# Kernel tuning notes

Measured on AMD Instinct MI355X. Metric: run time of the kernel, lower is better.

The kernel has to match this reference:

```python
import jax, jax.numpy as jnp
import numpy as np

B, T, S, L = 1, 2048, 512, 1024
C, H, Hk, D = 2048, 16, 4, 128
THETA = 10000.0


def setup_inputs() -> dict:
    key = jax.random.key(0)
    ks = jax.random.split(key, 9)
    sd = 0.02
    return {
        "x": jax.random.normal(ks[0], (B, T, C), jnp.float32),
        "stm": jax.random.normal(ks[1], (B, S, C), jnp.float32),
        "long_q": jax.random.normal(ks[2], (B, L, H, D), jnp.float32),
        "long_k": jax.random.normal(ks[3], (B, L, Hk, D), jnp.float32),
        "long_v": jax.random.normal(ks[4], (B, L, Hk, D), jnp.float32),
        "Wq": jax.random.normal(ks[5], (C, C), jnp.float32) * sd,
        "Wk": jax.random.normal(ks[6], (C, Hk * D), jnp.float32) * sd,
        "Wv": jax.random.normal(ks[7], (C, Hk * D), jnp.float32) * sd,
        "Wo": jax.random.normal(ks[8], (C, C), jnp.float32) * sd,
    }


def _rope_cos_sin(n, d, theta):
    # precompute_freqs_cis: freqs over even dims, angles t*freq
    freqs = 1.0 / (theta ** (jnp.arange(0, d, 2, dtype=jnp.float32) / d))
    ang = jnp.arange(n, dtype=jnp.float32)[:, None] * freqs[None, :]  # (n, d/2)
    return jnp.cos(ang), jnp.sin(ang)


def _apply_rope(x, cos, sin):
    # x: (B, n, h, D); complex-pair rotation over consecutive dims
    x1, x2 = x[..., 0::2], x[..., 1::2]
    c = cos[None, :, None, :]
    s = sin[None, :, None, :]
    r1 = x1 * c - x2 * s
    r2 = x1 * s + x2 * c
    return jnp.stack([r1, r2], axis=-1).reshape(x.shape)


def reference(x, stm, long_q, long_k, long_v, Wq, Wk, Wv, Wo):
    Bb, Tt, Cc = x.shape
    Ss, Ll = stm.shape[1], long_q.shape[1]
    seq = jnp.concatenate([stm, x], axis=1)  # (B, S+T, C)
    q = jnp.concatenate([long_q, (seq @ Wq).reshape(Bb, Ss + Tt, H, D)], axis=1)
    k = jnp.concatenate([long_k, (seq @ Wk).reshape(Bb, Ss + Tt, Hk, D)], axis=1)
    v = jnp.concatenate([long_v, (seq @ Wv).reshape(Bb, Ss + Tt, Hk, D)], axis=1)
    # inline RoPE on the last T+S positions only (memory bank keeps fixed encoding)
    cos, sin = _rope_cos_sin(Ss + Tt, D, THETA)
    q = q.at[:, Ll:].set(_apply_rope(q[:, Ll:], cos, sin))
    k = k.at[:, Ll:].set(_apply_rope(k[:, Ll:], cos, sin))
    tot = Ll + Ss + Tt
    # structured memory mask: causal over full stream, memory keys (< L+S) visible to all
    idx = jnp.arange(tot)
    mask = (idx[None, :] <= idx[:, None]) | (idx[None, :] < Ll + Ss)  # (tot, tot)
    # GQA: repeat_interleave kv heads
    rep = H // Hk
    kr = jnp.repeat(k, rep, axis=2)  # (B, tot, H, D)
    vr = jnp.repeat(v, rep, axis=2)
    att = jnp.einsum("bihd,bjhd->bhij", q, kr) * (1.0 / np.sqrt(D))
    att = jnp.where(mask[None, None], att, -jnp.inf)
    att = jax.nn.softmax(att, axis=-1)
    y = jnp.einsum("bhij,bjhd->bihd", att, vr).reshape(Bb, tot, Cc)
    y = y[:, -Tt:]  # keep only current-block outputs
    return y @ Wo
```

## Files before the change

kernel.cpp:

```cpp
#include <hip/hip_runtime.h>
#include <hip/hip_bf16.h>

typedef __attribute__((ext_vector_type(8))) short short8;
typedef __attribute__((ext_vector_type(4))) short short4v;
typedef __attribute__((ext_vector_type(4))) float f32x4;
typedef __attribute__((ext_vector_type(4))) float float4v;
typedef __attribute__((ext_vector_type(4))) int i32x4;

#define DEVFN static __device__ __forceinline__

#define T_N   2048
#define S_N   512
#define L_N   1024
#define C_N   2048
#define H_N   16
#define HK_N  4
#define D_N   128
#define ST_N  2560
#define TOT_N 3584
#define KV_N  512

DEVFN short f2bf(float f) {
  union { float f; unsigned u; } v; v.f = f;
  return (short)((v.u + 0x7FFFu + ((v.u >> 16) & 1u)) >> 16);
}
DEVFN float bf2f(short s) {
  union { unsigned u; float f; } v; v.u = ((unsigned)(unsigned short)s) << 16;
  return v.f;
}
DEVFN void gload16(const void* g, void* l) {
  __builtin_amdgcn_global_load_lds(
      (__attribute__((address_space(1))) void*)(g),
      (__attribute__((address_space(3))) void*)(l), 16, 0, 0);
}

#define Q_A (S_N * C_N / 4)
#define Q_B (Q_A + T_N * C_N / 4)
#define Q_C (Q_B + L_N * KV_N / 4)
#define Q_D (Q_C + L_N * KV_N / 4)
#define TAB_E (Q_D + ST_N * 64)
__global__ void k_setup(const float* __restrict__ x, const float* __restrict__ stm,
                        const float* __restrict__ lk, const float* __restrict__ lv,
                        short* __restrict__ seq, short* __restrict__ Kf,
                        short* __restrict__ Vf, float* __restrict__ ct,
                        float* __restrict__ st_) {
  int i = blockIdx.x * 256 + threadIdx.x;
  if (i < Q_D) {
    const float* src; short* dst; int off;
    if (i < Q_A)      { src = stm; dst = seq;                         off = i; }
    else if (i < Q_B) { src = x;   dst = seq + (size_t)S_N * C_N;     off = i - Q_A; }
    else if (i < Q_C) { src = lk;  dst = Kf;                          off = i - Q_B; }
    else              { src = lv;  dst = Vf;                          off = i - Q_C; }
    float4v v = reinterpret_cast<const float4v*>(src)[off];
    short4v o;
    o[0] = f2bf(v[0]); o[1] = f2bf(v[1]); o[2] = f2bf(v[2]); o[3] = f2bf(v[3]);
    reinterpret_cast<short4v*>(dst)[off] = o;
  } else {
    int j = i - Q_D;
    int p = j >> 6, fq = j & 63;
    float freq = expf(-(float)fq * (logf(10000.0f) / 64.0f));
    float ang = (float)p * freq;
    ct[j] = cosf(ang);
    st_[j] = sinf(ang);
  }
}

__global__ void k_tconv_all(const float* __restrict__ Wq, const float* __restrict__ Wk,
                            const float* __restrict__ Wv, const float* __restrict__ Wo,
                            short* __restrict__ WqT, short* __restrict__ WkT,
                            short* __restrict__ WvT, short* __restrict__ WoT) {
  __shared__ float tile[32][33];
  const int z = blockIdx.z;
  const float* in = (z == 0) ? Wq : (z == 1) ? Wk : (z == 2) ? Wv : Wo;
  short* outp     = (z == 0) ? WqT : (z == 1) ? WkT : (z == 2) ? WvT : WoT;
  const int cols = (z == 1 || z == 2) ? KV_N : C_N;
  if (blockIdx.x * 32 >= cols) return;
  int c0 = blockIdx.x * 32, r0 = blockIdx.y * 32;
  int tx = threadIdx.x, ty = threadIdx.y;
#pragma unroll
  for (int i = 0; i < 4; i++)
    tile[ty + i * 8][tx] = in[(size_t)(r0 + ty + i * 8) * cols + c0 + tx];
  __syncthreads();
#pragma unroll
  for (int i = 0; i < 4; i++)
    outp[(size_t)(c0 + ty + i * 8) * C_N + r0 + tx] = f2bf(tile[tx][ty + i * 8]);
}

__global__ void k_tv(const short* __restrict__ vf, short* __restrict__ vt) {
  __shared__ short tile[32][33];
  int hk = blockIdx.z;
  int r0 = blockIdx.x * 32;
  int d0 = blockIdx.y * 32;
  int tx = threadIdx.x, ty = threadIdx.y;
#pragma unroll
  for (int i = 0; i < 4; i++)
    tile[ty + i * 8][tx] = vf[(size_t)(r0 + ty + i * 8) * KV_N + hk * D_N + d0 + tx];
  __syncthreads();
  short* o = vt + (size_t)hk * D_N * TOT_N;
#pragma unroll
  for (int i = 0; i < 4; i++)
    o[(size_t)(d0 + ty + i * 8) * TOT_N + r0 + tx] = tile[tx][ty + i * 8];
}

__global__ __launch_bounds__(256) void k_gemm_o(
    const short* __restrict__ A, const short* __restrict__ Bt,
    float* __restrict__ C) {
  __shared__ short lbuf[2 * 6144];
  const int tid = threadIdx.x;
  const int w = tid >> 6, l = tid & 63;
  const int l15 = l & 15, lh = l >> 4;
  const int f0 = blockIdx.x;
  const int f = ((f0 & 7) << 6) + (f0 >> 3);
  const int rb = (f >> 4) << 6, cb = (f & 15) << 7;
  const int wr = (w >> 1) << 5, wc = (w & 1) << 6;
  f32x4 acc[2][4] = {};
  const int cA = tid;
  const short* pa = &A[(size_t)(rb + (cA >> 2)) * 2048 + (((cA ^ (cA >> 2)) & 3) << 3)];
  const int cB0 = tid, cB1 = 256 + tid;
  const short* pb0 = &Bt[(size_t)(cb + (cB0 >> 2)) * 2048 + (((cB0 ^ (cB0 >> 2)) & 3) << 3)];
  const short* pb1 = &Bt[(size_t)(cb + (cB1 >> 2)) * 2048 + (((cB1 ^ (cB1 >> 2)) & 3) << 3)];
  const int offA  = (w * 64) << 4;
  const int offB0 = 4096 + ((w * 64) << 4);
  const int offB1 = 4096 + ((256 + w * 64) << 4);
  char* lbase = (char*)lbuf;
  const int sw = (lh ^ (l15 & 3)) << 3;
  gload16(pa,  lbase + offA);
  gload16(pb0, lbase + offB0);
  gload16(pb1, lbase + offB1);
  int cur = 0;
  for (int kt = 0; kt < 2048; kt += 32) {
    const bool more = (kt + 32 < 2048);
    if (more) {
      char* p = lbase + (cur ^ 1) * 12288;
      gload16(pa  + kt + 32, p + offA);
      gload16(pb0 + kt + 32, p + offB0);
      gload16(pb1 + kt + 32, p + offB1);
      asm volatile("s_waitcnt vmcnt(3)" ::: "memory");
    } else {
      asm volatile("s_waitcnt vmcnt(0)" ::: "memory");
    }
    __builtin_amdgcn_s_barrier();
    __builtin_amdgcn_sched_barrier(0);
    const short* la = (const short*)(lbase + cur * 12288);
    const short* lb = (const short*)(lbase + cur * 12288 + 4096);
    short8 af[2], bg[4];
#pragma unroll
    for (int m = 0; m < 2; m++)
      af[m] = *reinterpret_cast<const short8*>(&la[(wr + m * 16 + l15) * 32 + sw]);
#pragma unroll
    for (int n = 0; n < 4; n++)
      bg[n] = *reinterpret_cast<const short8*>(&lb[(wc + n * 16 + l15) * 32 + sw]);
    __builtin_amdgcn_s_setprio(1);
#pragma unroll
    for (int m = 0; m < 2; m++)
#pragma unroll
      for (int n = 0; n < 4; n++)
        acc[m][n] = __builtin_amdgcn_mfma_f32_16x16x32_bf16(af[m], bg[n], acc[m][n], 0, 0, 0);
    __builtin_amdgcn_s_setprio(0);
    asm volatile("s_waitcnt lgkmcnt(0)" ::: "memory");
    __builtin_amdgcn_sched_barrier(0);
    __builtin_amdgcn_s_barrier();
    __builtin_amdgcn_sched_barrier(0);
    cur ^= 1;
  }
#pragma unroll
  for (int m = 0; m < 2; m++)
#pragma unroll
    for (int n = 0; n < 4; n++)
#pragma unroll
      for (int r = 0; r < 4; r++) {
        int row = rb + wr + m * 16 + lh * 4 + r;
        int col = cb + wc + n * 16 + l15;
        C[(size_t)row * 2048 + col] = acc[m][n][r];
      }
}

__global__ __launch_bounds__(256) void k_gemm_qkv(
    const short* __restrict__ A, const short* __restrict__ Bt,
    short* __restrict__ qbuf, short* __restrict__ Kf, short* __restrict__ Vf,
    const float* __restrict__ ct, const float* __restrict__ st_) {
  const int Kd = C_N;
  __shared__ short lbuf[2 * 2 * 4096];
  const int tid = threadIdx.x;
  const int w = tid >> 6, l = tid & 63;
  const int l15 = l & 15, lh = l >> 4;
  const int f0 = blockIdx.x;
  const int f = (f0 % 8) * 52 + f0 / 8;
  int rb, cb;
  if (f < 256) {
    rb = 512 + ((f >> 4) << 7);
    cb = (f & 15) << 7;
  } else {
    int g = f - 256;
    rb = (g >> 3) << 7;
    cb = 2048 + ((g & 7) << 7);
  }
  const int wr = (w >> 1) << 6, wc = (w & 1) << 6;
  f32x4 acc[4][4] = {};
  const int c0 = tid, c1 = 256 + tid;
  const short* pa0 = &A[(size_t)(rb + (c0 >> 2)) * Kd + (((c0 ^ (c0 >> 2)) & 3) << 3)];
  const short* pa1 = &A[(size_t)(rb + (c1 >> 2)) * Kd + (((c1 ^ (c1 >> 2)) & 3) << 3)];
  const short* pb0 = &Bt[(size_t)(cb + (c0 >> 2)) * Kd + (((c0 ^ (c0 >> 2)) & 3) << 3)];
  const short* pb1 = &Bt[(size_t)(cb + (c1 >> 2)) * Kd + (((c1 ^ (c1 >> 2)) & 3) << 3)];
  const int offA0 = (w * 64) << 4, offA1 = ((256 + w * 64) << 4);
  char* lbase = (char*)lbuf;
  const int sw = (lh ^ (l15 & 3)) << 3;
  {
    gload16(pa0, lbase + offA0);
    gload16(pa1, lbase + offA1);
    gload16(pb0, lbase + 8192 + offA0);
    gload16(pb1, lbase + 8192 + offA1);
  }
  int cur = 0;
  for (int kt = 0; kt < Kd; kt += 32) {
    const bool more = (kt + 32 < Kd);
    if (more) {
      char* p = lbase + ((cur ^ 1) << 14);
      gload16(pa0 + kt + 32, p + offA0);
      gload16(pa1 + kt + 32, p + offA1);
      gload16(pb0 + kt + 32, p + 8192 + offA0);
      gload16(pb1 + kt + 32, p + 8192 + offA1);
      asm volatile("s_waitcnt vmcnt(4)" ::: "memory");
    } else {
      asm volatile("s_waitcnt vmcnt(0)" ::: "memory");
    }
    __builtin_amdgcn_s_barrier();
    __builtin_amdgcn_sched_barrier(0);
    const short* la = (const short*)(lbase + (cur << 14));
    const short* lb = (const short*)(lbase + (cur << 14) + 8192);
    short8 af[4], bg[4];
#pragma unroll
    for (int m = 0; m < 4; m++)
      af[m] = *reinterpret_cast<const short8*>(&la[(wr + m * 16 + l15) * 32 + sw]);
#pragma unroll
    for (int n = 0; n < 4; n++)
      bg[n] = *reinterpret_cast<const short8*>(&lb[(wc + n * 16 + l15) * 32 + sw]);
    __builtin_amdgcn_s_setprio(1);
#pragma unroll
    for (int m = 0; m < 4; m++)
#pragma unroll
      for (int n = 0; n < 4; n++)
        acc[m][n] = __builtin_amdgcn_mfma_f32_16x16x32_bf16(af[m], bg[n], acc[m][n], 0, 0, 0);
    __builtin_amdgcn_s_setprio(0);
    asm volatile("s_waitcnt lgkmcnt(0)" ::: "memory");
    __builtin_amdgcn_sched_barrier(0);
    __builtin_amdgcn_s_barrier();
    __builtin_amdgcn_sched_barrier(0);
    cur ^= 1;
  }
#pragma unroll
  for (int m = 0; m < 4; m++)
#pragma unroll
    for (int n = 0; n < 4; n++) {
      int coln = cb + wc + n * 16 + l15;
      const bool do_rope = coln < 2560;
      const int fidx = (coln & 127) >> 1;
#pragma unroll
      for (int r = 0; r < 4; r++) {
        int row = rb + wr + m * 16 + lh * 4 + r;
        float v = acc[m][n][r];
        float other = __shfl_xor(v, 1, 64);
        if (do_rope) {
          float co = ct[row * 64 + fidx];
          float si = st_[row * 64 + fidx];
          v = (l15 & 1) ? (other * si + v * co) : (v * co - other * si);
        }
        short bv = f2bf(v);
        if (coln < 2048) {
          if (row >= 512) qbuf[(size_t)(row - 512) * C_N + coln] = bv;
        } else if (coln < 2560) {
          Kf[(size_t)(L_N + row) * KV_N + (coln - 2048)] = bv;
        } else {
          Vf[(size_t)(L_N + row) * KV_N + (coln - 2560)] = bv;
        }
      }
    }
}

__global__ __launch_bounds__(256, 2) void k_attn(
    const short* __restrict__ Q,
    const short* __restrict__ Kf,
    const short* __restrict__ Vt,
    short* __restrict__ pY,
    float* __restrict__ pM,
    float* __restrict__ pL) {
  __shared__ short kl[64 * 128];
  __shared__ short vl[128 * 64];
  const int f = blockIdx.x;
  const int p = f >> 8;
  const int f8 = f & 255;
  const int hk = f8 & 3;
  const int qraw = (f8 >> 2) & 15;
  const int hh = (f8 >> 6) & 3;
  const int qb = p ? (15 - qraw) : qraw;
  const int h = hk * 4 + hh;
  const int tid = threadIdx.x, w = tid >> 6, l = tid & 63;
  const int l15 = l & 15, lh = l >> 4;
  const int qbase = qb << 7;
  const int qrow0 = qbase + (w << 5);
  short8 aqA[4], aqB[4];
#pragma unroll
  for (int kb = 0; kb < 4; kb++) {
    aqA[kb] = *reinterpret_cast<const short8*>(
        &Q[(size_t)(qrow0 + l15) * C_N + h * D_N + kb * 32 + lh * 8]);
    aqB[kb] = *reinterpret_cast<const short8*>(
        &Q[(size_t)(qrow0 + 16 + l15) * C_N + h * D_N + kb * 32 + lh * 8]);
  }
  short8 ones;
#pragma unroll
  for (int j = 0; j < 8; j++) ones[j] = (short)0x3F80;
  f32x4 yA[8] = {}, yB[8] = {};
  f32x4 lA_ = {}, lB_ = {};
  float mA = -3.0e38f, mB = -3.0e38f;
  const float K2 = 0.12751744f;
  const float THR = 90.0f;
  const int nkt = ((qbase + 1663) >> 6) + 1;
  const int th = nkt >> 1;
  const int t0 = p ? th : 0;
  const int t1 = p ? nkt : th;
  const short* psk[4];
  const short* psv[4];
  int ldsoff[4];
#pragma unroll
  for (int it = 0; it < 4; it++) {
    int c = it * 256 + tid;
    int kr = c >> 4, kkc = c & 15;
    int pkr = (kr & 0x23) | ((kr & 0x0C) << 1) | ((kr >> 2) & 4);
    psk[it] = &Kf[(size_t)pkr * KV_N + hk * D_N + ((kkc ^ (kr & 7)) << 3)];
    int vrow = c >> 3, vkc = c & 7;
    psv[it] = &Vt[(size_t)hk * D_N * TOT_N + (size_t)vrow * TOT_N + ((vkc ^ (vrow & 7)) << 3)];
    ldsoff[it] = (it * 256 + w * 64) << 4;
  }
#pragma unroll
  for (int it = 0; it < 4; it++)
    gload16(psk[it] + (size_t)t0 * 64 * KV_N, (char*)kl + ldsoff[it]);
#pragma unroll
  for (int it = 0; it < 4; it++)
    gload16(psv[it] + (size_t)t0 * 64, (char*)vl + ldsoff[it]);
  __syncthreads();
  for (int t = t0; t < t1; t++) {
    const bool more = (t + 1 < t1);
    short8 kreg[4], vreg[4];
    if (more) {
#pragma unroll
      for (int it = 0; it < 4; it++)
        kreg[it] = *reinterpret_cast<const short8*>(psk[it] + (size_t)(t + 1) * 64 * KV_N);
#pragma unroll
      for (int it = 0; it < 4; it++)
        vreg[it] = *reinterpret_cast<const short8*>(psv[it] + (size_t)(t + 1) * 64);
    }
    f32x4 sA[4] = {}, sB[4] = {};
    __builtin_amdgcn_s_setprio(1);
#pragma unroll
    for (int g = 0; g < 4; g++) {
      int row = g * 16 + l15;
#pragma unroll
      for (int kb = 0; kb < 4; kb++) {
        short8 bk = *reinterpret_cast<const short8*>(
            (const char*)kl + row * 256 + ((((kb << 2) + lh) ^ (row & 7)) << 4));
        sA[g] = __builtin_amdgcn_mfma_f32_16x16x32_bf16(bk, aqA[kb], sA[g], 0, 0, 0);
        sB[g] = __builtin_amdgcn_mfma_f32_16x16x32_bf16(bk, aqB[kb], sB[g], 0, 0, 0);
      }
    }
    __builtin_amdgcn_s_setprio(0);
    if ((t * 64 + 63) > (1536 + qrow0)) {
      int qi = qrow0 + l15;
#pragma unroll
      for (int g = 0; g < 4; g++)
#pragma unroll
        for (int r = 0; r < 4; r++) {
          int key = t * 64 + ((g >> 1) << 5) + (lh << 3) + ((g & 1) << 2) + r;
          if (key > 1536 + qi) sA[g][r] = -3.0e38f;
        }
    }
    if ((t * 64 + 63) > (1536 + qrow0 + 16)) {
      int qi = qrow0 + 16 + l15;
#pragma unroll
      for (int g = 0; g < 4; g++)
#pragma unroll
        for (int r = 0; r < 4; r++) {
          int key = t * 64 + ((g >> 1) << 5) + (lh << 3) + ((g & 1) << 2) + r;
          if (key > 1536 + qi) sB[g][r] = -3.0e38f;
        }
    }
    {
      float lm = sA[0][0];
#pragma unroll
      for (int g = 0; g < 4; g++)
#pragma unroll
        for (int r = 0; r < 4; r++) lm = fmaxf(lm, sA[g][r]);
      if (!__all(lm <= mA + THR)) {
        float rm = fmaxf(lm, __shfl_xor(lm, 16, 64));
        rm = fmaxf(rm, __shfl_xor(rm, 32, 64));
        float mn = fmaxf(mA, rm);
        float scf = __builtin_amdgcn_exp2f((mA - mn) * K2);
        mA = mn;
#pragma unroll
        for (int r = 0; r < 4; r++) {
          float sc_c = __shfl(scf, lh * 4 + r, 64);
          lA_[r] *= sc_c;
#pragma unroll
          for (int dg = 0; dg < 8; dg++) yA[dg][r] *= sc_c;
        }
      }
    }
    {
      float lm = sB[0][0];
#pragma unroll
      for (int g = 0; g < 4; g++)
#pragma unroll
        for (int r = 0; r < 4; r++) lm = fmaxf(lm, sB[g][r]);
      if (!__all(lm <= mB + THR)) {
        float rm = fmaxf(lm, __shfl_xor(lm, 16, 64));
        rm = fmaxf(rm, __shfl_xor(rm, 32, 64));
        float mn = fmaxf(mB, rm);
        float scf = __builtin_amdgcn_exp2f((mB - mn) * K2);
        mB = mn;
#pragma unroll
        for (int r = 0; r < 4; r++) {
          float sc_c = __shfl(scf, lh * 4 + r, 64);
          lB_[r] *= sc_c;
#pragma unroll
          for (int dg = 0; dg < 8; dg++) yB[dg][r] *= sc_c;
        }
      }
    }
    union { i32x4 wv; short8 sv; } uA0, uA1, uB0, uB1;
    {
      const float mk = mA * K2;
      float pvv[16];
#pragma unroll
      for (int g = 0; g < 4; g++)
#pragma unroll
        for (int r = 0; r < 4; r++)
          pvv[g * 4 + r] = __builtin_amdgcn_exp2f(sA[g][r] * K2 - mk);
#pragma unroll
      for (int j = 0; j < 4; j++) {
        unsigned w0, w1;
        int b0 = (j >> 1) * 4 + 2 * (j & 1);
        int b1 = (2 + (j >> 1)) * 4 + 2 * (j & 1);
        asm("v_cvt_pk_bf16_f32 %0, %1, %2" : "=v"(w0) : "v"(pvv[b0]), "v"(pvv[b0 + 1]));
        asm("v_cvt_pk_bf16_f32 %0, %1, %2" : "=v"(w1) : "v"(pvv[b1]), "v"(pvv[b1 + 1]));
        uA0.wv[j] = (int)w0;
        uA1.wv[j] = (int)w1;
      }
    }
    {
      const float mk = mB * K2;
      float pvv[16];
#pragma unroll
      for (int g = 0; g < 4; g++)
#pragma unroll
        for (int r = 0; r < 4; r++)
          pvv[g * 4 + r] = __builtin_amdgcn_exp2f(sB[g][r] * K2 - mk);
#pragma unroll
      for (int j = 0; j < 4; j++) {
        unsigned w0, w1;
        int b0 = (j >> 1) * 4 + 2 * (j & 1);
        int b1 = (2 + (j >> 1)) * 4 + 2 * (j & 1);
        asm("v_cvt_pk_bf16_f32 %0, %1, %2" : "=v"(w0) : "v"(pvv[b0]), "v"(pvv[b0 + 1]));
        asm("v_cvt_pk_bf16_f32 %0, %1, %2" : "=v"(w1) : "v"(pvv[b1]), "v"(pvv[b1 + 1]));
        uB0.wv[j] = (int)w0;
        uB1.wv[j] = (int)w1;
      }
    }
    lA_ = __builtin_amdgcn_mfma_f32_16x16x32_bf16(uA0.sv, ones, lA_, 0, 0, 0);
    lA_ = __builtin_amdgcn_mfma_f32_16x16x32_bf16(uA1.sv, ones, lA_, 0, 0, 0);
    lB_ = __builtin_amdgcn_mfma_f32_16x16x32_bf16(uB0.sv, ones, lB_, 0, 0, 0);
    lB_ = __builtin_amdgcn_mfma_f32_16x16x32_bf16(uB1.sv, ones, lB_, 0, 0, 0);
    __builtin_amdgcn_s_setprio(1);
#pragma unroll
    for (int dg = 0; dg < 8; dg++) {
      int vrow = dg * 16 + l15;
      short8 bv0 = *reinterpret_cast<const short8*>(
          (const char*)vl + (vrow << 7) + ((lh ^ (vrow & 7)) << 4));
      short8 bv1 = *reinterpret_cast<const short8*>(
          (const char*)vl + (vrow << 7) + (((4 + lh) ^ (vrow & 7)) << 4));
      yA[dg] = __builtin_amdgcn_mfma_f32_16x16x32_bf16(uA0.sv, bv0, yA[dg], 0, 0, 0);
      yA[dg] = __builtin_amdgcn_mfma_f32_16x16x32_bf16(uA1.sv, bv1, yA[dg], 0, 0, 0);
      yB[dg] = __builtin_amdgcn_mfma_f32_16x16x32_bf16(uB0.sv, bv0, yB[dg], 0, 0, 0);
      yB[dg] = __builtin_amdgcn_mfma_f32_16x16x32_bf16(uB1.sv, bv1, yB[dg], 0, 0, 0);
    }
    __builtin_amdgcn_s_setprio(0);
    asm volatile("s_waitcnt lgkmcnt(0)" ::: "memory");
    __builtin_amdgcn_sched_barrier(0);
    __builtin_amdgcn_s_barrier();
    __builtin_amdgcn_sched_barrier(0);
    if (more) {
#pragma unroll
      for (int it = 0; it < 4; it++)
        *reinterpret_cast<short8*>((char*)kl + ldsoff[it] + (l << 4)) = kreg[it];
#pragma unroll
      for (int it = 0; it < 4; it++)
        *reinterpret_cast<short8*>((char*)vl + ldsoff[it] + (l << 4)) = vreg[it];
    }
    __syncthreads();
  }
  const size_t base = (size_t)(p * 16 + h) * 2048;
#pragma unroll
  for (int dg = 0; dg < 8; dg++)
#pragma unroll
    for (int r = 0; r < 4; r++) {
      int rowA = qrow0 + lh * 4 + r;
      pY[(base + rowA) * 128 + dg * 16 + l15] = f2bf(yA[dg][r]);
      pY[(base + rowA + 16) * 128 + dg * 16 + l15] = f2bf(yB[dg][r]);
    }
  if (l15 == 0) {
#pragma unroll
    for (int r = 0; r < 4; r++) {
      pL[base + qrow0 + lh * 4 + r] = lA_[r];
      pL[base + qrow0 + 16 + lh * 4 + r] = lB_[r];
    }
  }
  if (lh == 0) {
    pM[base + qrow0 + l15] = mA;
    pM[base + qrow0 + 16 + l15] = mB;
  }
}

__global__ void k_merge(const short* __restrict__ pY, const float* __restrict__ pM,
                        const float* __restrict__ pL, short* __restrict__ Y) {
  const int h = blockIdx.y;
  const int row = blockIdx.x * 16 + (threadIdx.x >> 4);
  const int d0 = (threadIdx.x & 15) * 8;
  const size_t b0 = (size_t)h * 2048 + row;
  const size_t b1 = (size_t)(16 + h) * 2048 + row;
  const float K2 = 0.12751744f;
  float m0 = pM[b0], m1 = pM[b1];
  float l0 = pL[b0], l1 = pL[b1];
  float M = fmaxf(m0, m1);
  float a0 = __builtin_amdgcn_exp2f((m0 - M) * K2);
  float a1 = __builtin_amdgcn_exp2f((m1 - M) * K2);
  float inv = 1.0f / (l0 * a0 + l1 * a1);
  short8 y0 = *reinterpret_cast<const short8*>(&pY[b0 * 128 + d0]);
  short8 y1 = *reinterpret_cast<const short8*>(&pY[b1 * 128 + d0]);
  short8 o;
#pragma unroll
  for (int j = 0; j < 8; j++)
    o[j] = f2bf((bf2f(y0[j]) * a0 + bf2f(y1[j]) * a1) * inv);
  *reinterpret_cast<short8*>(&Y[(size_t)row * C_N + h * D_N + d0]) = o;
}

extern "C" void kernel_launch(void* const* d_in, const int* in_sizes, int n_in,
                              void* d_out, int out_size, void* d_ws, size_t ws_size,
                              hipStream_t stream) {
  const float* x      = (const float*)d_in[0];
  const float* stm    = (const float*)d_in[1];
  const float* long_k = (const float*)d_in[3];
  const float* long_v = (const float*)d_in[4];
  const float* Wq     = (const float*)d_in[5];
  const float* Wk     = (const float*)d_in[6];
  const float* Wv     = (const float*)d_in[7];
  const float* Wo     = (const float*)d_in[8];
  float* out = (float*)d_out;

  short* seq  = (short*)d_ws;
  short* WqT  = seq  + (size_t)ST_N * C_N;
  short* WkT  = WqT  + (size_t)C_N * C_N;
  short* WvT  = WkT  + (size_t)KV_N * C_N;
  short* WoT  = WvT  + (size_t)KV_N * C_N;
  short* qbuf = WoT  + (size_t)C_N * C_N;
  short* Kf   = qbuf + (size_t)T_N * C_N;
  short* Vf   = Kf   + (size_t)TOT_N * KV_N;
  short* Vt   = Vf   + (size_t)TOT_N * KV_N;
  short* ybuf = Vt   + (size_t)TOT_N * KV_N;
  float* ctab = (float*)(ybuf + (size_t)T_N * C_N);
  float* stab = ctab + (size_t)ST_N * 64;

  short* pY = (short*)d_ws;
  float* pM = (float*)(pY + (size_t)2 * 16 * 2048 * 128);
  float* pL = pM + (size_t)2 * 16 * 2048;

  k_setup<<<TAB_E / 256, 256, 0, stream>>>(x, stm, long_k, long_v, seq, Kf, Vf, ctab, stab);

  k_tconv_all<<<dim3(64, 64, 4), dim3(32, 8), 0, stream>>>(
      Wq, Wk, Wv, Wo, WqT, WkT, WvT, WoT);

  k_gemm_qkv<<<416, 256, 0, stream>>>(seq, WqT, qbuf, Kf, Vf, ctab, stab);

  k_tv<<<dim3(TOT_N / 32, D_N / 32, HK_N), dim3(32, 8), 0, stream>>>(Vf, Vt);

  k_attn<<<512, 256, 0, stream>>>(qbuf, Kf, Vt, pY, pM, pL);

  k_merge<<<dim3(128, 16), 256, 0, stream>>>(pY, pM, pL, ybuf);

  k_gemm_o<<<512, 256, 0, stream>>>(ybuf, WoT, out);
}
```

Baseline: 169.3 us.

## Split attention KV range four ways and merge four partial softmax results

The attention kernel now divides each query block's key tiles into four chunks instead of two, launching 1024 blocks, and the merge kernel combines four partial outputs using their max and sum statistics. The launch bound is raised to allow four blocks per CU. Two of the partial output buffers are placed in the output buffer as scratch, because the output is only written later by the O-projection GEMM. More blocks gives better load balance and occupancy, at the cost of more partial-result traffic, a heavier merge, and possible register spills under the tighter launch bound.

```diff
diff --git a/kernel.cpp b/kernel.cpp
--- a/kernel.cpp
+++ b/kernel.cpp
@@ -277,11 +277,12 @@
     }
 }
 
-__global__ __launch_bounds__(256, 2) void k_attn(
+__global__ __launch_bounds__(256, 4) void k_attn(
     const short* __restrict__ Q,
     const short* __restrict__ Kf,
     const short* __restrict__ Vt,
-    short* __restrict__ pY,
+    short* __restrict__ pYa,
+    short* __restrict__ pYb,
     float* __restrict__ pM,
     float* __restrict__ pL) {
   __shared__ short kl[64 * 128];
@@ -292,7 +293,7 @@
   const int hk = f8 & 3;
   const int qraw = (f8 >> 2) & 15;
   const int hh = (f8 >> 6) & 3;
-  const int qb = p ? (15 - qraw) : qraw;
+  const int qb = (p & 1) ? (15 - qraw) : qraw;
   const int h = hk * 4 + hh;
   const int tid = threadIdx.x, w = tid >> 6, l = tid & 63;
   const int l15 = l & 15, lh = l >> 4;
@@ -315,9 +316,8 @@
   const float K2 = 0.12751744f;
   const float THR = 90.0f;
   const int nkt = ((qbase + 1663) >> 6) + 1;
-  const int th = nkt >> 1;
-  const int t0 = p ? th : 0;
-  const int t1 = p ? nkt : th;
+  const int tb = (p * nkt) >> 2;
+  const int te = ((p + 1) * nkt) >> 2;
   const short* psk[4];
   const short* psv[4];
   int ldsoff[4];
@@ -333,13 +333,13 @@
   }
 #pragma unroll
   for (int it = 0; it < 4; it++)
-    gload16(psk[it] + (size_t)t0 * 64 * KV_N, (char*)kl + ldsoff[it]);
+    gload16(psk[it] + (size_t)tb * 64 * KV_N, (char*)kl + ldsoff[it]);
 #pragma unroll
   for (int it = 0; it < 4; it++)
-    gload16(psv[it] + (size_t)t0 * 64, (char*)vl + ldsoff[it]);
+    gload16(psv[it] + (size_t)tb * 64, (char*)vl + ldsoff[it]);
   __syncthreads();
-  for (int t = t0; t < t1; t++) {
-    const bool more = (t + 1 < t1);
+  for (int t = tb; t < te; t++) {
+    const bool more = (t + 1 < te);
     short8 kreg[4], vreg[4];
     if (more) {
 #pragma unroll
@@ -496,48 +496,64 @@
     }
     __syncthreads();
   }
-  const size_t base = (size_t)(p * 16 + h) * 2048;
+  short* py = (p < 2) ? (pYa + (size_t)p * 16 * 2048 * 128)
+                      : (pYb + (size_t)(p - 2) * 16 * 2048 * 128);
+  const size_t baseY = (size_t)h * 2048;
+  const size_t baseML = (size_t)(p * 16 + h) * 2048;
 #pragma unroll
   for (int dg = 0; dg < 8; dg++)
 #pragma unroll
     for (int r = 0; r < 4; r++) {
       int rowA = qrow0 + lh * 4 + r;
-      pY[(base + rowA) * 128 + dg * 16 + l15] = f2bf(yA[dg][r]);
-      pY[(base + rowA + 16) * 128 + dg * 16 + l15] = f2bf(yB[dg][r]);
+      py[(baseY + rowA) * 128 + dg * 16 + l15] = f2bf(yA[dg][r]);
+      py[(baseY + rowA + 16) * 128 + dg * 16 + l15] = f2bf(yB[dg][r]);
     }
   if (l15 == 0) {
 #pragma unroll
     for (int r = 0; r < 4; r++) {
-      pL[base + qrow0 + lh * 4 + r] = lA_[r];
-      pL[base + qrow0 + 16 + lh * 4 + r] = lB_[r];
+      pL[baseML + qrow0 + lh * 4 + r] = lA_[r];
+      pL[baseML + qrow0 + 16 + lh * 4 + r] = lB_[r];
     }
   }
   if (lh == 0) {
-    pM[base + qrow0 + l15] = mA;
-    pM[base + qrow0 + 16 + l15] = mB;
-  }
-}
-
-__global__ void k_merge(const short* __restrict__ pY, const float* __restrict__ pM,
-                        const float* __restrict__ pL, short* __restrict__ Y) {
+    pM[baseML + qrow0 + l15] = mA;
+    pM[baseML + qrow0 + 16 + l15] = mB;
+  }
+}
+
+__global__ void k_merge(const short* __restrict__ pYa, const short* __restrict__ pYb,
+                        const float* __restrict__ pM, const float* __restrict__ pL,
+                        short* __restrict__ Y) {
   const int h = blockIdx.y;
   const int row = blockIdx.x * 16 + (threadIdx.x >> 4);
   const int d0 = (threadIdx.x & 15) * 8;
-  const size_t b0 = (size_t)h * 2048 + row;
-  const size_t b1 = (size_t)(16 + h) * 2048 + row;
   const float K2 = 0.12751744f;
-  float m0 = pM[b0], m1 = pM[b1];
-  float l0 = pL[b0], l1 = pL[b1];
-  float M = fmaxf(m0, m1);
-  float a0 = __builtin_amdgcn_exp2f((m0 - M) * K2);
-  float a1 = __builtin_amdgcn_exp2f((m1 - M) * K2);
-  float inv = 1.0f / (l0 * a0 + l1 * a1);
-  short8 y0 = *reinterpret_cast<const short8*>(&pY[b0 * 128 + d0]);
-  short8 y1 = *reinterpret_cast<const short8*>(&pY[b1 * 128 + d0]);
+  float m[4], lv[4];
+#pragma unroll
+  for (int i = 0; i < 4; i++) {
+    m[i]  = pM[(size_t)(i * 16 + h) * 2048 + row];
+    lv[i] = pL[(size_t)(i * 16 + h) * 2048 + row];
+  }
+  float M = fmaxf(fmaxf(m[0], m[1]), fmaxf(m[2], m[3]));
+  float a[4], den = 0.0f;
+#pragma unroll
+  for (int i = 0; i < 4; i++) {
+    a[i] = __builtin_amdgcn_exp2f((m[i] - M) * K2);
+    den += lv[i] * a[i];
+  }
+  float inv = 1.0f / den;
+  float acc[8] = {};
+#pragma unroll
+  for (int i = 0; i < 4; i++) {
+    const short* py = (i < 2) ? (pYa + (size_t)i * 16 * 2048 * 128)
+                              : (pYb + (size_t)(i - 2) * 16 * 2048 * 128);
+    short8 y = *reinterpret_cast<const short8*>(&py[((size_t)h * 2048 + row) * 128 + d0]);
+#pragma unroll
+    for (int j = 0; j < 8; j++) acc[j] += bf2f(y[j]) * a[i];
+  }
   short8 o;
 #pragma unroll
-  for (int j = 0; j < 8; j++)
-    o[j] = f2bf((bf2f(y0[j]) * a0 + bf2f(y1[j]) * a1) * inv);
+  for (int j = 0; j < 8; j++) o[j] = f2bf(acc[j] * inv);
   *reinterpret_cast<short8*>(&Y[(size_t)row * C_N + h * D_N + d0]) = o;
 }
 
@@ -567,9 +583,10 @@
   float* ctab = (float*)(ybuf + (size_t)T_N * C_N);
   float* stab = ctab + (size_t)ST_N * 64;
 
-  short* pY = (short*)d_ws;
-  float* pM = (float*)(pY + (size_t)2 * 16 * 2048 * 128);
-  float* pL = pM + (size_t)2 * 16 * 2048;
+  short* pYa = (short*)d_ws;
+  float* pM  = (float*)(pYa + (size_t)2 * 16 * 2048 * 128);
+  float* pL  = pM + (size_t)4 * 16 * 2048;
+  short* pYb = (short*)d_out;
 
   k_setup<<<TAB_E / 256, 256, 0, stream>>>(x, stm, long_k, long_v, seq, Kf, Vf, ctab, stab);
 
@@ -580,9 +597,9 @@
 
   k_tv<<<dim3(TOT_N / 32, D_N / 32, HK_N), dim3(32, 8), 0, stream>>>(Vf, Vt);
 
-  k_attn<<<512, 256, 0, stream>>>(qbuf, Kf, Vt, pY, pM, pL);
-
-  k_merge<<<dim3(128, 16), 256, 0, stream>>>(pY, pM, pL, ybuf);
+  k_attn<<<1024, 256, 0, stream>>>(qbuf, Kf, Vt, pYa, pYb, pM, pL);
+
+  k_merge<<<dim3(128, 16), 256, 0, stream>>>(pYa, pYb, pM, pL, ybuf);
 
   k_gemm_o<<<512, 256, 0, stream>>>(ybuf, WoT, out);
 }
```

Measured after the change: 388.7 us. 130% more time.
